# Kernel optimization log

Measured on AMD Instinct MI355X. Metric: run time of the kernel, lower is better.

## Reference

```python
import jax, jax.numpy as jnp
import numpy as np

B, T = 256, 1024
IN_DIM, OUT_DIM = 32, 32
STATE_DIM, DIM_NL = 128, 128
EPS = 1e-3            # pos_def_tol
ALPHA = 1.0           # contraction_rate_lb
STD = 0.5             # initialization_std


def setup_inputs() -> dict:
    key = jax.random.key(0)
    ks = jax.random.split(key, 9)
    f = lambda k, sh: jax.random.normal(k, sh, dtype=jnp.float32)
    n, q = STATE_DIM, DIM_NL
    return {
        "x0_sys": f(ks[0], (B, 1, OUT_DIM)),
        "u_in": f(ks[1], (B, T, IN_DIM)),
        "X": f(ks[2], (2 * n + q, 2 * n + q)) * STD,
        "Y": f(ks[3], (n, n)) * STD,
        "B2": f(ks[4], (n, IN_DIM)) * STD,
        "C2": f(ks[5], (OUT_DIM, n)) * STD,
        "D21": f(ks[6], (OUT_DIM, q)) * STD,
        "D22": f(ks[7], (OUT_DIM, IN_DIM)) * STD,
        "D12": f(ks[8], (q, IN_DIM)) * STD,
    }


def _derived(X, Y):
    # Contraction-preserving reparametrization ("_update_model_param").
    n, q = STATE_DIM, DIM_NL
    H = X.T @ X + EPS * jnp.eye(2 * n + q, dtype=X.dtype)
    H11 = H[:n, :n]
    H21 = H[n:n + q, :n]
    H22 = H[n:n + q, n:n + q]
    H31 = H[n + q:, :n]
    H32 = H[n + q:, n:n + q]
    H33 = H[n + q:, n + q:]          # P
    F_ = H31
    B1 = H32
    E = 0.5 * (H11 + ALPHA * H33 + Y - Y.T)
    E_inv = jnp.linalg.inv(E)
    Lam = 0.5 * jnp.diag(H22)
    D11 = -jnp.tril(H22, -1)          # strictly lower triangular
    C1 = -H21
    return F_, B1, E_inv, Lam, D11, C1


def reference(x0_sys, u_in, X, Y, B2, C2, D21, D22, D12):
    F_, B1, E_inv, Lam, D11, C1 = _derived(X, Y)
    q = DIM_NL

    # reset(): x0 = min-norm lstsq solution of C2 x0 = y0_sys  (lstsq == pinv here)
    y0_sys = x0_sys[:, 0, :]                       # (B, out)
    x0 = (jnp.linalg.pinv(C2) @ y0_sys.T).T        # (B, n)
    y0 = x0 @ C2.T                                 # (B, out)

    idx = jnp.arange(q)

    def step(x, u):
        # one REN forward step; x:(B,n), u:(B,in)
        a = x @ C1.T + u @ D12.T                   # (B, q), i-independent part of v

        def inner(w, inp):
            i, d_row, lam, a_i = inp               # a_i:(B,)
            v = a_i + w @ d_row                    # strictly-lower-tri recurrence on w
            return w.at[:, i].set(jnp.tanh(v / lam)), None

        w0 = jnp.zeros((x.shape[0], q), x.dtype)
        w, _ = jax.lax.scan(inner, w0, (idx, D11, Lam, a.T))
        x_new = (x @ F_.T + w @ B1.T + u @ B2.T) @ E_inv.T
        y = x_new @ C2.T + w @ D21.T + u @ D22.T
        return x_new, y

    _, ys = jax.lax.scan(step, x0, jnp.swapaxes(u_in, 0, 1))   # (T, B, out)
    # run() emits y0 then outputs after u[0..T-2] (last step's y is dropped)
    y_traj = jnp.concatenate([y0[None], ys[:-1]], axis=0)      # (T, B, out)
    return jnp.swapaxes(y_traj, 0, 1)                          # (B, T, out)
```

## Files before the change

### kernel.cpp

```cpp
#include <hip/hip_runtime.h>
#include <hip/hip_bf16.h>

#define DEV static __device__ __forceinline__

constexpr int Tn = 1024;
constexpr float LOG2E = 1.4426950408889634f;

constexpr int OFF_H     = 0;
constexpr int OFF_E     = 147456;
constexpr int OFF_EINV  = 163840;
constexpr int OFF_M     = 180224;
constexpr int OFF_MINV  = 181248;
constexpr int OFF_GL2   = 182272;
constexpr int OFF_FH    = 182400;
constexpr int OFF_B1H   = 198784;
constexpr int OFF_B2H   = 215168;
constexpr int OFF_W0    = 219264;
constexpr int OFF_WC    = 223360;
constexpr int OFF_CF    = 227456;
constexpr int OFF_CB    = 243840;
constexpr int OFF_CB2   = 260224;
constexpr int OFF_PF    = 264320;
constexpr int OFF_PB    = 280704;
constexpr int OFF_PCF   = 297088;
constexpr int OFF_PCB   = 313472;
constexpr int OFF_SAB   = 329856;
constexpr int OFF_SB2   = 338048;
constexpr int OFF_BUQ   = 342144;
constexpr int OFF_D12Q  = 346240;
constexpr int OFF_SCB2  = 350336;
constexpr int OFF_WCS   = 354432;
constexpr int OFF_C2Y   = 358528;
constexpr int OFF_D21Y  = 362624;
constexpr int OFF_D22Y  = 366720;
constexpr int OFF_AUG   = 367744;
constexpr int OFF_AUG2  = 400512;
constexpr int OFF_X0    = 402560;
constexpr int OFF_A0    = 435328;
constexpr int WS_FLOATS = 468096;

__device__ __align__(16) float g_ws[WS_FLOATS];
__device__ int g_isf32;

DEV float ld(const void* p, size_t i, int f) {
  return f ? ((const float*)p)[i]
           : __bfloat162float(((const __hip_bfloat16*)p)[i]);
}
DEV float rdlane(float v, int l) {
  return __int_as_float(__builtin_amdgcn_readlane(__float_as_int(v), l));
}

__global__ void k_detect(const void* __restrict__ X) {
  if (threadIdx.x == 0) {
    const __hip_bfloat16* p = (const __hip_bfloat16*)X;
    int bad = 0;
    for (int i = 0; i < 512; ++i) {
      float v = __bfloat162float(p[i]);
      if (!(v > -1e6f && v < 1e6f)) bad++;
    }
    g_isf32 = (bad > 0) ? 1 : 0;
  }
}

__global__ void k_H(const void* __restrict__ X) {
  const int f = g_isf32;
  float* ws = g_ws;
  int id = blockIdx.x * 256 + threadIdx.x;
  int r = id / 384, c = id % 384;
  float acc = 0.f;
  for (int k = 0; k < 384; ++k)
    acc = fmaf(ld(X, k * 384 + r, f), ld(X, k * 384 + c, f), acc);
  if (r == c) acc += 0.001f;
  ws[OFF_H + id] = acc;
}

__global__ void k_derived(const void* __restrict__ Y, const void* __restrict__ C2) {
  const int f = g_isf32;
  float* ws = g_ws;
  const float* H = ws + OFF_H;
  int id = blockIdx.x * 256 + threadIdx.x;
  if (id < 16384) {
    int i = id >> 7, j = id & 127;
    ws[OFF_E + id] = 0.5f * (H[i * 384 + j] + H[(256 + i) * 384 + 256 + j]
                             + ld(Y, i * 128 + j, f) - ld(Y, j * 128 + i, f));
  } else if (id < 16512) {
    int i = id - 16384;
    ws[OFF_GL2 + i] = LOG2E * 4.f / H[(128 + i) * 384 + 128 + i];
  } else if (id < 17536) {
    int t = id - 16512; int a = t >> 5, b = t & 31;
    float acc = 0.f;
    for (int j = 0; j < 128; ++j)
      acc = fmaf(ld(C2, a * 128 + j, f), ld(C2, b * 128 + j, f), acc);
// ... 121 lines not shown
  if (id < 16384) {
    int l = id >> 7, j = id & 127;
    float a = 0.f;
    for (int m = 0; m < 128; ++m) a = fmaf(einv[l * 128 + m], H[(256 + m) * 384 + j], a);
    ws[OFF_FH + id] = a;
  } else if (id < 32768) {
    int t = id - 16384; int l = t >> 7, j = t & 127;
    float a = 0.f;
    for (int m = 0; m < 128; ++m) a = fmaf(einv[l * 128 + m], H[(256 + m) * 384 + 128 + j], a);
    ws[OFF_B1H + t] = a;
  } else if (id < 36864) {
    int t = id - 32768; int l = t >> 5, k = t & 31;
    float a = 0.f;
    for (int m = 0; m < 128; ++m) a = fmaf(einv[l * 128 + m], ld(B2, m * 32 + k, f), a);
    ws[OFF_B2H + t] = a;
  } else if (id < 40960) {
    int t = id - 36864; int k = t >> 7, l = t & 127;
    float a = 0.f;
    for (int m = 0; m < 32; ++m) a = fmaf(minv[k * 32 + m], ld(C2, m * 128 + l, f), a);
    ws[OFF_W0 + t] = a;
  }
}

__global__ void k_w2() {
  float* ws = g_ws;
  const float* H = ws + OFF_H;
  const float* w0 = ws + OFF_W0;
  int id = blockIdx.x * 256 + threadIdx.x;
  int k = id >> 7, l = id & 127;
  float a = 0.f;
  for (int m = 0; m < 128; ++m) a = fmaf(w0[k * 128 + m], -H[(128 + l) * 384 + m], a);
  ws[OFF_WC + id] = a;
}

__global__ void k_cf() {
  float* ws = g_ws;
  const float* H = ws + OFF_H;
  int id = blockIdx.x * 256 + threadIdx.x;
  if (id < 16384) {
    int l = id >> 7, j = id & 127;
    float a = 0.f;
    for (int m = 0; m < 128; ++m) a = fmaf(-H[(128 + l) * 384 + m], ws[OFF_FH + m * 128 + j], a);
    ws[OFF_CF + id] = a;
  } else if (id < 32768) {
    int t = id - 16384; int l = t >> 7, j = t & 127;
    float a = 0.f;
    for (int m = 0; m < 128; ++m) a = fmaf(-H[(128 + l) * 384 + m], ws[OFF_B1H + m * 128 + j], a);
    ws[OFF_CB + t] = a;
  } else {
    int t = id - 32768; int l = t >> 5, k = t & 31;
    float a = 0.f;
    for (int m = 0; m < 128; ++m) a = fmaf(-H[(128 + l) * 384 + m], ws[OFF_B2H + m * 32 + k], a);
    ws[OFF_CB2 + t] = a;
  }
}

__global__ void k_pk(const void* __restrict__ D12, const void* __restrict__ C2,
                     const void* __restrict__ D21, const void* __restrict__ D22) {
  const int f = g_isf32;
  float* ws = g_ws;
  const float* H = ws + OFF_H;
  const float* g = ws + OFF_GL2;
  int id = blockIdx.x * 256 + threadIdx.x;
  if (id < 8192) {
    int j = id >> 6, l = id & 63;
    ((float2*)(ws + OFF_PF))[id] =
        make_float2(ws[OFF_FH + l * 128 + j], ws[OFF_FH + (l + 64) * 128 + j]);
  } else if (id < 16384) {
    int t = id - 8192; int j = t >> 6, l = t & 63;
    ((float2*)(ws + OFF_PB))[t] =
        make_float2(ws[OFF_B1H + l * 128 + j], ws[OFF_B1H + (l + 64) * 128 + j]);
  } else if (id < 24576) {
    int t = id - 16384; int j = t >> 6, l = t & 63;
    ((float2*)(ws + OFF_PCF))[t] =
        make_float2(g[l] * ws[OFF_CF + l * 128 + j], g[l + 64] * ws[OFF_CF + (l + 64) * 128 + j]);
  } else if (id < 32768) {
    int t = id - 24576; int j = t >> 6, l = t & 63;
    ((float2*)(ws + OFF_PCB))[t] =
        make_float2(g[l] * ws[OFF_CB + l * 128 + j], g[l + 64] * ws[OFF_CB + (l + 64) * 128 + j]);
  } else if (id < 36864) {
    int t = id - 32768; int i = t >> 6, l = t & 63;
    float sx = (i < l) ? -g[l] * H[(128 + l) * 384 + 128 + i] : 0.f;
    float sy = -g[l + 64] * H[(192 + l) * 384 + 128 + i];
    ((float2*)(ws + OFF_SAB))[t] = make_float2(sx, sy);
  } else if (id < 40960) {
    int t = id - 36864; int ii = t >> 6, l = t & 63;
    ws[OFF_SB2 + t] = (ii < l) ? -g[l + 64] * H[(192 + l) * 384 + 192 + ii] : 0.f;
  } else if (id < 43008) {
    int t = id - 40960; int k = t >> 6, l = t & 63;
    ((float2*)(ws + OFF_BUQ))[t] =
        make_float2(ws[OFF_B2H + l * 32 + k], ws[OFF_B2H + (l + 64) * 32 + k]);
  } else if (id < 45056) {
    int t = id - 43008; int k = t >> 6, l = t & 63;
    ((float2*)(ws + OFF_D12Q))[t] =
        make_float2(g[l] * ld(D12, l * 32 + k, f), g[l + 64] * ld(D12, (l + 64) * 32 + k, f));
  } else if (id < 47104) {
    int t = id - 45056; int k = t >> 6, l = t & 63;
    ((float2*)(ws + OFF_SCB2))[t] =
        make_float2(g[l] * ws[OFF_CB2 + l * 32 + k], g[l + 64] * ws[OFF_CB2 + (l + 64) * 32 + k]);
  } else if (id < 49152) {
    int t = id - 47104; int k = t >> 6, l = t & 63;
    ((float2*)(ws + OFF_WCS))[t] =
        make_float2(g[l] * ws[OFF_WC + k * 128 + l], g[l + 64] * ws[OFF_WC + k * 128 + l + 64]);
  } else if (id < 53248) {
    int t = id - 49152; int m = t >> 5, o = t & 31;
    ws[OFF_C2Y + t] = ld(C2, o * 128 + m, f);
  } else if (id < 57344) {
    int t = id - 53248; int m = t >> 5, o = t & 31;
    ws[OFF_D21Y + t] = ld(D21, o * 128 + m, f);
  } else if (id < 58368) {
    int t = id - 57344; int k = t >> 5, o = t & 31;
    ws[OFF_D22Y + t] = ld(D22, o * 32 + k, f);
  }
}

__global__ void k_x0a0(const void* __restrict__ x0s, const void* __restrict__ u_in) {
  const int f = g_isf32;
  float* ws = g_ws;
  int id = blockIdx.x * 256 + threadIdx.x;
  if (id < 32768) {
    int b = id >> 7, l = id & 127;
    float a = 0.f;
    for (int k = 0; k < 32; ++k)
      a = fmaf(ld(x0s, b * 32 + k, f), ws[OFF_W0 + k * 128 + l], a);
    ws[OFF_X0 + id] = a;
  } else {
    int t = id - 32768; int b = t >> 6, lane = t & 63;
    const float2* WCs = (const float2*)(ws + OFF_WCS);
    const float2* D12Q = (const float2*)(ws + OFF_D12Q);
    float ax = 0.f, ay = 0.f;
    for (int k = 0; k < 32; ++k) {
      float yk = ld(x0s, b * 32 + k, f);
      float2 wc = WCs[k * 64 + lane];
      ax = fmaf(wc.x, yk, ax); ay = fmaf(wc.y, yk, ay);
      float u0 = ld(u_in, b * Tn * 32 + k, f);
      float2 dq = D12Q[k * 64 + lane];
      ax = fmaf(dq.x, u0, ax); ay = fmaf(dq.y, u0, ay);
    }
    ((float2*)(ws + OFF_A0))[b * 64 + lane] = make_float2(ax, ay);
  }
}

DEV void y_emit(const float* ws, float xlv, float xhv, float2 wv, float uyv,
                int b, int t, int lane, int f, void* out) {
  int o = lane & 31, h = lane >> 5;
  const float* C2Y = ws + OFF_C2Y;
  const float* D21Y = ws + OFF_D21Y;
  const float* D22Y = ws + OFF_D22Y;
  float acc = 0.f;
#pragma unroll 8
  for (int l = 0; l < 64; ++l) {
    float xle = rdlane(xlv, l), xhe = rdlane(xhv, l);
    float xv = h ? xhe : xle;
    acc = fmaf(xv, C2Y[(l + 64 * h) * 32 + o], acc);
  }
#pragma unroll 8
  for (int l = 0; l < 64; ++l) {
    float wxe = rdlane(wv.x, l), wye = rdlane(wv.y, l);
    float wvv = h ? wye : wxe;
    acc = fmaf(wvv, D21Y[(l + 64 * h) * 32 + o], acc);
  }
  if (h == 0) {
#pragma unroll 8
    for (int k = 0; k < 32; ++k)
      acc = fmaf(rdlane(uyv, k), D22Y[k * 32 + o], acc);
  }
  acc += __shfl_down(acc, 32);
  if (lane < 32) {
    size_t oi = ((size_t)b * Tn + t) * 32 + o;
    if (f) ((float*)out)[oi] = acc;
    else   ((__hip_bfloat16*)out)[oi] = __float2bfloat16(acc);
  }
}

DEV void y_emit_l(const float* sC2Y, const float* sD21Y, const float* sD22Y,
                  float xlv, float xhv, float2 wv, float uyv,
                  int b, int t, int lane, int f, void* out) {
  int o = lane & 31, h = lane >> 5;
  float acc = 0.f;
#pragma unroll 8
  for (int l = 0; l < 64; ++l) {
    float xle = rdlane(xlv, l), xhe = rdlane(xhv, l);
    float xv = h ? xhe : xle;
    acc = fmaf(xv, sC2Y[(l + 64 * h) * 32 + o], acc);
  }
#pragma unroll 8
  for (int l = 0; l < 64; ++l) {
    float wxe = rdlane(wv.x, l), wye = rdlane(wv.y, l);
    float wvv = h ? wye : wxe;
    acc = fmaf(wvv, sD21Y[(l + 64 * h) * 32 + o], acc);
  }
  if (h == 0) {
#pragma unroll 8
    for (int k = 0; k < 32; ++k)
      acc = fmaf(rdlane(uyv, k), sD22Y[k * 32 + o], acc);
  }
  acc += __shfl_down(acc, 32);
  if (lane < 32) {
    size_t oi = ((size_t)b * Tn + t) * 32 + o;
    if (f) ((float*)out)[oi] = acc;
    else   ((__hip_bfloat16*)out)[oi] = __float2bfloat16(acc);
  }
}

__global__ __launch_bounds__(512, 2) void k_scan8m(const void* __restrict__ u_in,
                                                   const void* __restrict__ x0s,
                                                   void* __restrict__ out) {
  extern __shared__ float sm[];
  float2* sSAB  = (float2*)sm;
  float*  sSB2  = sm + 8192;
  float2* xbuf  = (float2*)(sm + 12288);
  float2* abuf  = (float2*)(sm + 14336);
  float2* wbuf  = (float2*)(sm + 16384);
  float2* sBUQ  = (float2*)(sm + 16640);
  float2* sSCB2 = (float2*)(sm + 20736);
  float2* sD12Q = (float2*)(sm + 24832);
  float*  sC2Y  = sm + 28928;
  float*  sD21Y = sm + 33024;
  float*  sD22Y = sm + 37120;
  const float* ws = g_ws;
  const int f = g_isf32;
  const int tid = threadIdx.x, lane = tid & 63, w = tid >> 6;
  for (int i = tid; i < 4096; i += 512) sSAB[i] = ((const float2*)(ws + OFF_SAB))[i];
  for (int i = tid; i < 4096; i += 512) sSB2[i] = ws[OFF_SB2 + i];
  for (int i = tid; i < 2048; i += 512) sBUQ[i] = ((const float2*)(ws + OFF_BUQ))[i];
  for (int i = tid; i < 2048; i += 512) sSCB2[i] = ((const float2*)(ws + OFF_SCB2))[i];
  for (int i = tid; i < 2048; i += 512) sD12Q[i] = ((const float2*)(ws + OFF_D12Q))[i];
  for (int i = tid; i < 4096; i += 512) sC2Y[i] = ws[OFF_C2Y + i];
  for (int i = tid; i < 4096; i += 512) sD21Y[i] = ws[OFF_D21Y + i];
  for (int i = tid; i < 1024; i += 512) sD22Y[i] = ws[OFF_D22Y + i];

  const int b = blockIdx.x;
  const bool isScan = (w < 4);

  float2 vA[32], vB[32];
  {
    const float2* P1 = (const float2*)(ws + (isScan ? OFF_PB : OFF_PF));
    const float2* P2 = (const float2*)(ws + (isScan ? OFF_PCB : OFF_PCF));
    const int jcol = (w & 3) * 32;
#pragma unroll
    for (int c = 0; c < 32; ++c) {
      vA[c] = P1[(jcol + c) * 64 + lane];
      vB[c] = P2[(jcol + c) * 64 + lane];
    }
  }
  float xl = ws[OFF_X0 + b * 128 + lane];
  float xh = ws[OFF_X0 + b * 128 + 64 + lane];
  float accx = 0.f, accy = 0.f;
  if (isScan) {
    float2 a2 = ((const float2*)(ws + OFF_A0))[b * 64 + lane];
    accx = a2.x; accy = a2.y;
  }
  float ucur = 0.f;
  float u0v = 0.f, u1v = 0.f;
  float uyc = 0.f;
  if (w == 4 && lane < 32) ucur = ld(u_in, (size_t)b * Tn * 32 + lane, f);
  if (w == 5 && lane < 32) {
    u0v = ld(u_in, (size_t)b * Tn * 32 + lane, f);
    u1v = ld(u_in, ((size_t)b * Tn + 1) * 32 + lane, f);
  }
  if (w == 7 && lane < 32) {
    size_t oi = (size_t)b * Tn * 32 + lane;
    float v = ld(x0s, b * 32 + lane, f);
    if (f) ((float*)out)[oi] = v;
    else   ((__hip_bfloat16*)out)[oi] = __float2bfloat16(v);
  }
  const int jb = __builtin_amdgcn_readfirstlane((w & 1) * 32);
  __syncthreads();

#pragma unroll 1
  for (int t = 0; t < Tn - 1; ++t) {
    const int p = t & 1;
    if (isScan) {
      __builtin_amdgcn_s_setprio(1);
      float s = rdlane(accx, 0);
#pragma unroll
      for (int i = 0; i < 64; ++i) {
        float e2 = __builtin_amdgcn_exp2f(s);
        float r  = __builtin_amdgcn_rcpf(1.f + e2);
        float wi = fmaf(-2.f, r, 1.f);
        float2 sp = sSAB[i * 64 + lane];
        if (i < 63) {
          float spn  = rdlane(sp.x, i + 1);
          float sold = rdlane(accx, i + 1);
          s = fmaf(spn, wi, sold);
        }
        accx = fmaf(sp.x, wi, accx);
        accy = fmaf(sp.y, wi, accy);
      }
      float ex = __builtin_amdgcn_exp2f(accx);
      float wxv = fmaf(-2.f, __builtin_amdgcn_rcpf(1.f + ex), 1.f);
      float s2 = rdlane(accy, 0);
#pragma unroll
      for (int i = 0; i < 64; ++i) {
        float e2 = __builtin_amdgcn_exp2f(s2);
        float r  = __builtin_amdgcn_rcpf(1.f + e2);
        float wi = fmaf(-2.f, r, 1.f);
        float sb = sSB2[i * 64 + lane];
        if (i < 63) {
          float spn  = rdlane(sb, i + 1);
          float sold = rdlane(accy, i + 1);
          s2 = fmaf(spn, wi, sold);
        }
        accy = fmaf(sb, wi, accy);
      }
      float ey = __builtin_amdgcn_exp2f(accy);
      float wyv = fmaf(-2.f, __builtin_amdgcn_rcpf(1.f + ey), 1.f);
      if (w == 0) wbuf[p * 64 + lane] = make_float2(wxv, wyv);

      float px = 0.f, py = 0.f, pax = 0.f, pay = 0.f;
      float wsrc = (w < 2) ? wxv : wyv;
#pragma unroll
      for (int c = 0; c < 32; ++c) {
        float wj = rdlane(wsrc, jb + c);
        px  = fmaf(vA[c].x, wj, px);
        py  = fmaf(vA[c].y, wj, py);
        pax = fmaf(vB[c].x, wj, pax);
        pay = fmaf(vB[c].y, wj, pay);
      }
      __builtin_amdgcn_s_setprio(0);
      xbuf[(p * 8 + w) * 64 + lane] = make_float2(px, py);
      abuf[(p * 8 + w) * 64 + lane] = make_float2(pax, pay);
      __syncthreads();
      float sax = 0.f, say = 0.f;
#pragma unroll
      for (int w2 = 0; w2 < 8; ++w2) {
        float2 av = abuf[(p * 8 + w2) * 64 + lane];
        sax += av.x; say += av.y;
      }
      accx = sax; accy = say;
    } else {
      float px = 0.f, py = 0.f, pax = 0.f, pay = 0.f;
      if (w == 4) {
        float un = ucur;
        if (lane < 32) un = ld(u_in, ((size_t)b * Tn + t + 1) * 32 + lane, f);
#pragma unroll 8
        for (int k = 0; k < 32; ++k) {
          float uk = rdlane(ucur, k);
          float2 bu = sBUQ[k * 64 + lane];
          px = fmaf(bu.x, uk, px); py = fmaf(bu.y, uk, py);
        }
        ucur = un;
      } else if (w == 5) {
        float u2v = u1v;
        if (lane < 32 && t + 2 < Tn) u2v = ld(u_in, ((size_t)b * Tn + t + 2) * 32 + lane, f);
#pragma unroll 8
        for (int k = 0; k < 32; ++k) {
          float u0k = rdlane(u0v, k);
          float2 sc = sSCB2[k * 64 + lane];
          pax = fmaf(sc.x, u0k, pax); pay = fmaf(sc.y, u0k, pay);
          float u1k = rdlane(u1v, k);
          float2 dq = sD12Q[k * 64 + lane];
          pax = fmaf(dq.x, u1k, pax); pay = fmaf(dq.y, u1k, pay);
        }
        u0v = u1v; u1v = u2v;
      } else if (w == 7) {
        float uyn = uyc;
        if (lane < 32) uyn = ld(u_in, ((size_t)b * Tn + t) * 32 + lane, f);
        if (t >= 1) {
          float2 wv = wbuf[((t - 1) & 1) * 64 + lane];
          y_emit_l(sC2Y, sD21Y, sD22Y, xl, xh, wv, uyc, b, t, lane, f, out);
        }
        uyc = uyn;
      }
      float xsrc = (w < 6) ? xl : xh;
#pragma unroll
      for (int c = 0; c < 32; ++c) {
        float xj = rdlane(xsrc, jb + c);
        px  = fmaf(vA[c].x, xj, px);
        py  = fmaf(vA[c].y, xj, py);
        pax = fmaf(vB[c].x, xj, pax);
        pay = fmaf(vB[c].y, xj, pay);
      }
      xbuf[(p * 8 + w) * 64 + lane] = make_float2(px, py);
      abuf[(p * 8 + w) * 64 + lane] = make_float2(pax, pay);
      __syncthreads();
      float sxl = 0.f, sxh = 0.f;
#pragma unroll
      for (int w2 = 0; w2 < 8; ++w2) {
        float2 xv = xbuf[(p * 8 + w2) * 64 + lane];
        sxl += xv.x; sxh += xv.y;
      }
      xl = sxl; xh = sxh;
    }
  }
  if (w == 7) {
    float2 wv = wbuf[((Tn - 2) & 1) * 64 + lane];
    y_emit_l(sC2Y, sD21Y, sD22Y, xl, xh, wv, uyc, b, Tn - 1, lane, f, out);
  }
}

__global__ __launch_bounds__(512) void k_scan8_fb(const void* __restrict__ u_in,
                                                  const void* __restrict__ x0s,
                                                  void* __restrict__ out) {
  __shared__ float2 sSAB[64 * 64];
  __shared__ float  sSB2[64 * 64];
  __shared__ float2 xbuf[2][8][64];
  __shared__ float2 abuf[2][8][64];
  const float* ws = g_ws;
  const int f = g_isf32;
  const int tid = threadIdx.x, lane = tid & 63, w = tid >> 6;
  for (int i = tid; i < 4096; i += 512) sSAB[i] = ((const float2*)(ws + OFF_SAB))[i];
  for (int i = tid; i < 4096; i += 512) sSB2[i] = ws[OFF_SB2 + i];

  const int b = blockIdx.x;
  const bool isScan = (w < 4);
  float2 vA[32], vB[32];
  if (isScan) {
    const float2* P1 = (const float2*)(ws + OFF_PB);
    const float2* P2 = (const float2*)(ws + OFF_PCB);
    const int jcol = (w & 3) * 32;
#pragma unroll
    for (int c = 0; c < 32; ++c) {
      vA[c] = P1[(jcol + c) * 64 + lane];
      vB[c] = P2[(jcol + c) * 64 + lane];
    }
  }
  float xl = ws[OFF_X0 + b * 128 + lane];
  float xh = ws[OFF_X0 + b * 128 + 64 + lane];
  float2 a2 = ((const float2*)(ws + OFF_A0))[b * 64 + lane];
  float accx = a2.x, accy = a2.y;
  float ucur = 0.f;
  float u0v = 0.f, u1v = 0.f;
  float uyc = 0.f;
  if (w == 4 && lane < 32) ucur = ld(u_in, (size_t)b * Tn * 32 + lane, f);
  if (w == 6 && lane < 32) {
    u0v = ld(u_in, (size_t)b * Tn * 32 + lane, f);
    u1v = ld(u_in, ((size_t)b * Tn + 1) * 32 + lane, f);
  }
  if (w == 6) { xbuf[0][6][lane] = make_float2(0.f, 0.f); xbuf[1][6][lane] = make_float2(0.f, 0.f); }
  if (w == 7 && lane < 32) {
    size_t oi = (size_t)b * Tn * 32 + lane;
    float v = ld(x0s, b * 32 + lane, f);
    if (f) ((float*)out)[oi] = v;
    else   ((__hip_bfloat16*)out)[oi] = __float2bfloat16(v);
  }
  const int jb = __builtin_amdgcn_readfirstlane((w & 1) * 32);
  __syncthreads();

#pragma unroll 1
  for (int t = 0; t < Tn - 1; ++t) {
// ... 77 lines not shown
      xl = sxl; xh = sxh;
    } else if (w == 5) {
      float px = 0.f, py = 0.f, pax = 0.f, pay = 0.f;
      const float2* PF = (const float2*)(ws + OFF_PF);
      const float2* PCF = (const float2*)(ws + OFF_PCF);
#pragma unroll 8
      for (int c = 0; c < 64; ++c) {
        float xj = rdlane(xh, c);
        float2 fv = PF[(64 + c) * 64 + lane];
        float2 cv = PCF[(64 + c) * 64 + lane];
        px  = fmaf(fv.x, xj, px);  py  = fmaf(fv.y, xj, py);
        pax = fmaf(cv.x, xj, pax); pay = fmaf(cv.y, xj, pay);
      }
      xbuf[p][5][lane] = make_float2(px, py);
      abuf[p][5][lane] = make_float2(pax, pay);
      __syncthreads();
      float sxl = 0.f, sxh = 0.f;
#pragma unroll
      for (int w2 = 0; w2 < 7; ++w2) {
        float2 xv = xbuf[p][w2][lane];
        sxl += xv.x; sxh += xv.y;
      }
      xl = sxl; xh = sxh;
    } else if (w == 6) {
      float u2v = u1v;
      if (lane < 32 && t + 2 < Tn) u2v = ld(u_in, ((size_t)b * Tn + t + 2) * 32 + lane, f);
      float pax = 0.f, pay = 0.f;
      const float2* SC = (const float2*)(ws + OFF_SCB2);
      const float2* DQ = (const float2*)(ws + OFF_D12Q);
#pragma unroll 8
      for (int k = 0; k < 32; ++k) {
        float u0k = rdlane(u0v, k);
        float2 sc = SC[k * 64 + lane];
        pax = fmaf(sc.x, u0k, pax); pay = fmaf(sc.y, u0k, pay);
        float u1k = rdlane(u1v, k);
        float2 dq = DQ[k * 64 + lane];
        pax = fmaf(dq.x, u1k, pax); pay = fmaf(dq.y, u1k, pay);
      }
      u0v = u1v; u1v = u2v;
      abuf[p][6][lane] = make_float2(pax, pay);
      __syncthreads();
      float sxl = 0.f, sxh = 0.f;
#pragma unroll
      for (int w2 = 0; w2 < 7; ++w2) {
        float2 xv = xbuf[p][w2][lane];
        sxl += xv.x; sxh += xv.y;
      }
      xl = sxl; xh = sxh;
    } else {
      float uyn = uyc;
      if (lane < 32) uyn = ld(u_in, ((size_t)b * Tn + t) * 32 + lane, f);
      if (t >= 1) {
        float2 wv = xbuf[(t - 1) & 1][7][lane];
        y_emit(ws, xl, xh, wv, uyc, b, t, lane, f, out);
      }
      uyc = uyn;
      __syncthreads();
      float sxl = 0.f, sxh = 0.f;
#pragma unroll
      for (int w2 = 0; w2 < 7; ++w2) {
        float2 xv = xbuf[p][w2][lane];
        sxl += xv.x; sxh += xv.y;
      }
      xl = sxl; xh = sxh;
    }
  }
  if (w == 7) {
    float2 wv = xbuf[(Tn - 2) & 1][7][lane];
    y_emit(ws, xl, xh, wv, uyc, b, Tn - 1, lane, f, out);
  }
}

extern "C" void kernel_launch(void* const* d_in, const int* in_sizes, int n_in,
                              void* d_out, int out_size, void* d_ws, size_t ws_size,
                              hipStream_t stream) {
  const void* x0s = d_in[0];
  const void* u   = d_in[1];
  const void* X   = d_in[2];
  const void* Y   = d_in[3];
  const void* B2  = d_in[4];
  const void* C2  = d_in[5];
  const void* D21 = d_in[6];
  const void* D22 = d_in[7];
  const void* D12 = d_in[8];
  (void)d_ws; (void)ws_size; (void)in_sizes; (void)n_in; (void)out_size;

  hipLaunchKernelGGL(k_detect,  dim3(1),     dim3(64),   0, stream, X);
  hipLaunchKernelGGL(k_H,       dim3(576),   dim3(256),  0, stream, X);
  hipLaunchKernelGGL(k_derived, dim3(69),    dim3(256),  0, stream, Y, C2);

  hipError_t e = hipFuncSetAttribute((const void*)k_inv_lds,
                                     hipFuncAttributeMaxDynamicSharedMemorySize,
                                     139264);
  if (e == hipSuccess) {
    hipLaunchKernelGGL(k_inv_lds, dim3(1), dim3(1024), 139264, stream);
  } else {
    (void)hipGetLastError();
    hipLaunchKernelGGL(k_inv,     dim3(1), dim3(1024), 0, stream);
  }

  hipLaunchKernelGGL(k_fuse,    dim3(160),   dim3(256),  0, stream, B2, C2);
  hipLaunchKernelGGL(k_w2,      dim3(16),    dim3(256),  0, stream);
  hipLaunchKernelGGL(k_cf,      dim3(144),   dim3(256),  0, stream);
  hipLaunchKernelGGL(k_pk,      dim3(228),   dim3(256),  0, stream, D12, C2, D21, D22);
  hipLaunchKernelGGL(k_x0a0,    dim3(192),   dim3(256),  0, stream, x0s, u);

  hipError_t e2 = hipFuncSetAttribute((const void*)k_scan8m,
                                      hipFuncAttributeMaxDynamicSharedMemorySize,
                                      152576);
  if (e2 == hipSuccess) {
    hipLaunchKernelGGL(k_scan8m, dim3(256), dim3(512), 152576, stream, u, x0s, d_out);
  } else {
    (void)hipGetLastError();
    hipLaunchKernelGGL(k_scan8_fb, dim3(256), dim3(512), 0, stream, u, x0s, d_out);
  }
}
```

Baseline: 6.940 ms.

## Fold w-dependent terms into precomputed matrices so scan waves split critical path

Precomputes the products F·B1, CF·B1 and C2·B1+D21 so the state update and next-step pre-activation can be formed directly from the previous step's w and x. This lets the four non-scan waves compute the whole x update, while the scan waves only handle the w recurrence and its contribution to a, shortening the serial critical path. Weights move from registers into LDS or are streamed from global memory, trading register pressure and occupancy for extra memory traffic. The launch-bounds minimum-occupancy hint is removed and the LDS allocation shrinks.

```diff
diff --git a/kernel.cpp b/kernel.cpp
--- a/kernel.cpp
+++ b/kernel.cpp
@@ -37,7 +37,12 @@
 constexpr int OFF_AUG2  = 400512;
 constexpr int OFF_X0    = 402560;
 constexpr int OFF_A0    = 435328;
-constexpr int WS_FLOATS = 468096;
+constexpr int OFF_M1    = 468096;
+constexpr int OFF_M2    = 484480;
+constexpr int OFF_M3Y   = 500864;
+constexpr int OFF_PM1   = 504960;
+constexpr int OFF_PM2   = 521344;
+constexpr int WS_FLOATS = 537728;
 
 __device__ __align__(16) float g_ws[WS_FLOATS];
 __device__ int g_isf32;
@@ -265,6 +270,31 @@
     float a = 0.f;
     for (int m = 0; m < 128; ++m) a = fmaf(-H[(128 + l) * 384 + m], ws[OFF_B2H + m * 32 + k], a);
     ws[OFF_CB2 + t] = a;
+  }
+}
+
+__global__ void k_m(const void* __restrict__ C2, const void* __restrict__ D21) {
+  const int f = g_isf32;
+  float* ws = g_ws;
+  int id = blockIdx.x * 256 + threadIdx.x;
+  if (id < 16384) {
+    int l = id >> 7, j = id & 127;
+    float a = 0.f;
+    for (int m = 0; m < 128; ++m)
+      a = fmaf(ws[OFF_FH + l * 128 + m], ws[OFF_B1H + m * 128 + j], a);
+    ws[OFF_M1 + id] = a;
+  } else if (id < 32768) {
+    int t = id - 16384; int l = t >> 7, j = t & 127;
+    float a = 0.f;
+    for (int m = 0; m < 128; ++m)
+      a = fmaf(ws[OFF_CF + l * 128 + m], ws[OFF_B1H + m * 128 + j], a);
+    ws[OFF_M2 + t] = a;
+  } else {
+    int t = id - 32768; int m = t >> 5, o = t & 31;
+    float a = ld(D21, o * 128 + m, f);
+    for (int l = 0; l < 128; ++l)
+      a = fmaf(ld(C2, o * 128 + l, f), ws[OFF_B1H + l * 128 + m], a);
+    ws[OFF_M3Y + t] = a;
   }
 }
 
@@ -324,6 +354,14 @@
   } else if (id < 58368) {
     int t = id - 57344; int k = t >> 5, o = t & 31;
     ws[OFF_D22Y + t] = ld(D22, o * 32 + k, f);
+  } else if (id < 66560) {
+    int t = id - 58368; int j = t >> 6, l = t & 63;
+    ((float2*)(ws + OFF_PM1))[t] =
+        make_float2(ws[OFF_M1 + l * 128 + j], ws[OFF_M1 + (l + 64) * 128 + j]);
+  } else if (id < 74752) {
+    int t = id - 66560; int j = t >> 6, l = t & 63;
+    ((float2*)(ws + OFF_PM2))[t] =
+        make_float2(g[l] * ws[OFF_M2 + l * 128 + j], g[l + 64] * ws[OFF_M2 + (l + 64) * 128 + j]);
   }
 }
 
@@ -354,12 +392,10 @@
   }
 }
 
-DEV void y_emit(const float* ws, float xlv, float xhv, float2 wv, float uyv,
-                int b, int t, int lane, int f, void* out) {
+DEV void y_emit_p(const float* C2Y, const float* DY, const float* D22Y,
+                  float xlv, float xhv, float2 wv, float uyv,
+                  int b, int t, int lane, int f, void* out) {
   int o = lane & 31, h = lane >> 5;
-  const float* C2Y = ws + OFF_C2Y;
-  const float* D21Y = ws + OFF_D21Y;
-  const float* D22Y = ws + OFF_D22Y;
   float acc = 0.f;
 #pragma unroll 8
   for (int l = 0; l < 64; ++l) {
@@ -371,7 +407,7 @@
   for (int l = 0; l < 64; ++l) {
     float wxe = rdlane(wv.x, l), wye = rdlane(wv.y, l);
     float wvv = h ? wye : wxe;
-    acc = fmaf(wvv, D21Y[(l + 64 * h) * 32 + o], acc);
+    acc = fmaf(wvv, DY[(l + 64 * h) * 32 + o], acc);
   }
   if (h == 0) {
 #pragma unroll 8
@@ -386,77 +422,27 @@
   }
 }
 
-DEV void y_emit_l(const float* sC2Y, const float* sD21Y, const float* sD22Y,
-                  float xlv, float xhv, float2 wv, float uyv,
-                  int b, int t, int lane, int f, void* out) {
-  int o = lane & 31, h = lane >> 5;
-  float acc = 0.f;
-#pragma unroll 8
-  for (int l = 0; l < 64; ++l) {
-    float xle = rdlane(xlv, l), xhe = rdlane(xhv, l);
-    float xv = h ? xhe : xle;
-    acc = fmaf(xv, sC2Y[(l + 64 * h) * 32 + o], acc);
-  }
-#pragma unroll 8
-  for (int l = 0; l < 64; ++l) {
-    float wxe = rdlane(wv.x, l), wye = rdlane(wv.y, l);
-    float wvv = h ? wye : wxe;
-    acc = fmaf(wvv, sD21Y[(l + 64 * h) * 32 + o], acc);
-  }
-  if (h == 0) {
-#pragma unroll 8
-    for (int k = 0; k < 32; ++k)
-      acc = fmaf(rdlane(uyv, k), sD22Y[k * 32 + o], acc);
-  }
-  acc += __shfl_down(acc, 32);
-  if (lane < 32) {
-    size_t oi = ((size_t)b * Tn + t) * 32 + o;
-    if (f) ((float*)out)[oi] = acc;
-    else   ((__hip_bfloat16*)out)[oi] = __float2bfloat16(acc);
-  }
-}
-
-__global__ __launch_bounds__(512, 2) void k_scan8m(const void* __restrict__ u_in,
-                                                   const void* __restrict__ x0s,
-                                                   void* __restrict__ out) {
+__global__ __launch_bounds__(512) void k_scan9(const void* __restrict__ u_in,
+                                               const void* __restrict__ x0s,
+                                               void* __restrict__ out) {
   extern __shared__ float sm[];
-  float2* sSAB  = (float2*)sm;
-  float*  sSB2  = sm + 8192;
-  float2* xbuf  = (float2*)(sm + 12288);
-  float2* abuf  = (float2*)(sm + 14336);
-  float2* wbuf  = (float2*)(sm + 16384);
-  float2* sBUQ  = (float2*)(sm + 16640);
-  float2* sSCB2 = (float2*)(sm + 20736);
-  float2* sD12Q = (float2*)(sm + 24832);
-  float*  sC2Y  = sm + 28928;
-  float*  sD21Y = sm + 33024;
-  float*  sD22Y = sm + 37120;
+  float2* sSAB = (float2*)sm;
+  float*  sSB2 = sm + 8192;
+  float2* sPCB = (float2*)(sm + 12288);
+  float2* xbuf = (float2*)(sm + 28672);
+  float2* abuf = (float2*)(sm + 30720);
+  float2* wbuf = (float2*)(sm + 32768);
   const float* ws = g_ws;
   const int f = g_isf32;
   const int tid = threadIdx.x, lane = tid & 63, w = tid >> 6;
   for (int i = tid; i < 4096; i += 512) sSAB[i] = ((const float2*)(ws + OFF_SAB))[i];
   for (int i = tid; i < 4096; i += 512) sSB2[i] = ws[OFF_SB2 + i];
-  for (int i = tid; i < 2048; i += 512) sBUQ[i] = ((const float2*)(ws + OFF_BUQ))[i];
-  for (int i = tid; i < 2048; i += 512) sSCB2[i] = ((const float2*)(ws + OFF_SCB2))[i];
-  for (int i = tid; i < 2048; i += 512) sD12Q[i] = ((const float2*)(ws + OFF_D12Q))[i];
-  for (int i = tid; i < 4096; i += 512) sC2Y[i] = ws[OFF_C2Y + i];
-  for (int i = tid; i < 4096; i += 512) sD21Y[i] = ws[OFF_D21Y + i];
-  for (int i = tid; i < 1024; i += 512) sD22Y[i] = ws[OFF_D22Y + i];
+  for (int i = tid; i < 8192; i += 512) sPCB[i] = ((const float2*)(ws + OFF_PCB))[i];
+  if (tid < 128) wbuf[tid] = make_float2(0.f, 0.f);
 
   const int b = blockIdx.x;
   const bool isScan = (w < 4);
 
-  float2 vA[32], vB[32];
-  {
-    const float2* P1 = (const float2*)(ws + (isScan ? OFF_PB : OFF_PF));
-    const float2* P2 = (const float2*)(ws + (isScan ? OFF_PCB : OFF_PCF));
-    const int jcol = (w & 3) * 32;
-#pragma unroll
-    for (int c = 0; c < 32; ++c) {
-      vA[c] = P1[(jcol + c) * 64 + lane];
-      vB[c] = P2[(jcol + c) * 64 + lane];
-    }
-  }
   float xl = ws[OFF_X0 + b * 128 + lane];
   float xh = ws[OFF_X0 + b * 128 + 64 + lane];
   float accx = 0.f, accy = 0.f;
@@ -521,18 +507,17 @@
       float wyv = fmaf(-2.f, __builtin_amdgcn_rcpf(1.f + ey), 1.f);
       if (w == 0) wbuf[p * 64 + lane] = make_float2(wxv, wyv);
 
-      float px = 0.f, py = 0.f, pax = 0.f, pay = 0.f;
+      float pax = 0.f, pay = 0.f;
       float wsrc = (w < 2) ? wxv : wyv;
+      const int jcol = w * 32;
 #pragma unroll
       for (int c = 0; c < 32; ++c) {
         float wj = rdlane(wsrc, jb + c);
-        px  = fmaf(vA[c].x, wj, px);
-        py  = fmaf(vA[c].y, wj, py);
-        pax = fmaf(vB[c].x, wj, pax);
-        pay = fmaf(vB[c].y, wj, pay);
+        float2 cv = sPCB[(jcol + c) * 64 + lane];
+        pax = fmaf(cv.x, wj, pax);
+        pay = fmaf(cv.y, wj, pay);
       }
       __builtin_amdgcn_s_setprio(0);
-      xbuf[(p * 8 + w) * 64 + lane] = make_float2(px, py);
       abuf[(p * 8 + w) * 64 + lane] = make_float2(pax, pay);
       __syncthreads();
       float sax = 0.f, say = 0.f;
@@ -543,27 +528,31 @@
       }
       accx = sax; accy = say;
     } else {
+      float2 wprev = wbuf[(p ^ 1) * 64 + lane];
       float px = 0.f, py = 0.f, pax = 0.f, pay = 0.f;
       if (w == 4) {
         float un = ucur;
         if (lane < 32) un = ld(u_in, ((size_t)b * Tn + t + 1) * 32 + lane, f);
+        const float2* BUq = (const float2*)(ws + OFF_BUQ);
 #pragma unroll 8
         for (int k = 0; k < 32; ++k) {
           float uk = rdlane(ucur, k);
-          float2 bu = sBUQ[k * 64 + lane];
+          float2 bu = BUq[k * 64 + lane];
           px = fmaf(bu.x, uk, px); py = fmaf(bu.y, uk, py);
         }
         ucur = un;
       } else if (w == 5) {
         float u2v = u1v;
         if (lane < 32 && t + 2 < Tn) u2v = ld(u_in, ((size_t)b * Tn + t + 2) * 32 + lane, f);
+        const float2* SC = (const float2*)(ws + OFF_SCB2);
+        const float2* DQ = (const float2*)(ws + OFF_D12Q);
 #pragma unroll 8
         for (int k = 0; k < 32; ++k) {
           float u0k = rdlane(u0v, k);
-          float2 sc = sSCB2[k * 64 + lane];
+          float2 sc = SC[k * 64 + lane];
           pax = fmaf(sc.x, u0k, pax); pay = fmaf(sc.y, u0k, pay);
           float u1k = rdlane(u1v, k);
-          float2 dq = sD12Q[k * 64 + lane];
+          float2 dq = DQ[k * 64 + lane];
           pax = fmaf(dq.x, u1k, pax); pay = fmaf(dq.y, u1k, pay);
         }
         u0v = u1v; u1v = u2v;
@@ -571,26 +560,37 @@
         float uyn = uyc;
         if (lane < 32) uyn = ld(u_in, ((size_t)b * Tn + t) * 32 + lane, f);
         if (t >= 1) {
-          float2 wv = wbuf[((t - 1) & 1) * 64 + lane];
-          y_emit_l(sC2Y, sD21Y, sD22Y, xl, xh, wv, uyc, b, t, lane, f, out);
+          y_emit_p(ws + OFF_C2Y, ws + OFF_M3Y, ws + OFF_D22Y,
+                   xl, xh, wprev, uyc, b, t, lane, f, out);
         }
         uyc = uyn;
       }
       float xsrc = (w < 6) ? xl : xh;
-#pragma unroll
+      float wps  = (w < 6) ? wprev.x : wprev.y;
+      const int jc = (w - 4) * 32;
+      const float2* PFp  = (const float2*)(ws + OFF_PF);
+      const float2* PM1p = (const float2*)(ws + OFF_PM1);
+      const float2* PCFp = (const float2*)(ws + OFF_PCF);
+      const float2* PM2p = (const float2*)(ws + OFF_PM2);
+#pragma unroll 8
       for (int c = 0; c < 32; ++c) {
         float xj = rdlane(xsrc, jb + c);
-        px  = fmaf(vA[c].x, xj, px);
-        py  = fmaf(vA[c].y, xj, py);
-        pax = fmaf(vB[c].x, xj, pax);
-        pay = fmaf(vB[c].y, xj, pay);
+        float wj = rdlane(wps, jb + c);
+        float2 fv = PFp [(jc + c) * 64 + lane];
+        float2 mv = PM1p[(jc + c) * 64 + lane];
+        float2 cv = PCFp[(jc + c) * 64 + lane];
+        float2 nv = PM2p[(jc + c) * 64 + lane];
+        px  = fmaf(fv.x, xj, px);  py  = fmaf(fv.y, xj, py);
+        px  = fmaf(mv.x, wj, px);  py  = fmaf(mv.y, wj, py);
+        pax = fmaf(cv.x, xj, pax); pay = fmaf(cv.y, xj, pay);
+        pax = fmaf(nv.x, wj, pax); pay = fmaf(nv.y, wj, pay);
       }
       xbuf[(p * 8 + w) * 64 + lane] = make_float2(px, py);
       abuf[(p * 8 + w) * 64 + lane] = make_float2(pax, pay);
       __syncthreads();
       float sxl = 0.f, sxh = 0.f;
 #pragma unroll
-      for (int w2 = 0; w2 < 8; ++w2) {
+      for (int w2 = 4; w2 < 8; ++w2) {
         float2 xv = xbuf[(p * 8 + w2) * 64 + lane];
         sxl += xv.x; sxh += xv.y;
       }
@@ -599,7 +599,8 @@
   }
   if (w == 7) {
     float2 wv = wbuf[((Tn - 2) & 1) * 64 + lane];
-    y_emit_l(sC2Y, sD21Y, sD22Y, xl, xh, wv, uyc, b, Tn - 1, lane, f, out);
+    y_emit_p(ws + OFF_C2Y, ws + OFF_M3Y, ws + OFF_D22Y,
+             xl, xh, wv, uyc, b, Tn - 1, lane, f, out);
   }
 }
 
@@ -783,7 +784,8 @@
       if (lane < 32) uyn = ld(u_in, ((size_t)b * Tn + t) * 32 + lane, f);
       if (t >= 1) {
         float2 wv = xbuf[(t - 1) & 1][7][lane];
-        y_emit(ws, xl, xh, wv, uyc, b, t, lane, f, out);
+        y_emit_p(ws + OFF_C2Y, ws + OFF_D21Y, ws + OFF_D22Y,
+                 xl, xh, wv, uyc, b, t, lane, f, out);
       }
       uyc = uyn;
       __syncthreads();
@@ -798,7 +800,8 @@
   }
   if (w == 7) {
     float2 wv = xbuf[(Tn - 2) & 1][7][lane];
-    y_emit(ws, xl, xh, wv, uyc, b, Tn - 1, lane, f, out);
+    y_emit_p(ws + OFF_C2Y, ws + OFF_D21Y, ws + OFF_D22Y,
+             xl, xh, wv, uyc, b, Tn - 1, lane, f, out);
   }
 }
 
@@ -833,14 +836,15 @@
   hipLaunchKernelGGL(k_fuse,    dim3(160),   dim3(256),  0, stream, B2, C2);
   hipLaunchKernelGGL(k_w2,      dim3(16),    dim3(256),  0, stream);
   hipLaunchKernelGGL(k_cf,      dim3(144),   dim3(256),  0, stream);
-  hipLaunchKernelGGL(k_pk,      dim3(228),   dim3(256),  0, stream, D12, C2, D21, D22);
+  hipLaunchKernelGGL(k_m,       dim3(144),   dim3(256),  0, stream, C2, D21);
+  hipLaunchKernelGGL(k_pk,      dim3(292),   dim3(256),  0, stream, D12, C2, D21, D22);
   hipLaunchKernelGGL(k_x0a0,    dim3(192),   dim3(256),  0, stream, x0s, u);
 
-  hipError_t e2 = hipFuncSetAttribute((const void*)k_scan8m,
+  hipError_t e2 = hipFuncSetAttribute((const void*)k_scan9,
                                       hipFuncAttributeMaxDynamicSharedMemorySize,
-                                      152576);
+                                      132096);
   if (e2 == hipSuccess) {
-    hipLaunchKernelGGL(k_scan8m, dim3(256), dim3(512), 152576, stream, u, x0s, d_out);
+    hipLaunchKernelGGL(k_scan9, dim3(256), dim3(512), 132096, stream, u, x0s, d_out);
   } else {
     (void)hipGetLastError();
     hipLaunchKernelGGL(k_scan8_fb, dim3(256), dim3(512), 0, stream, u, x0s, d_out);
```

Measured after the change: 14.97 ms. +115.7%, slower.

## Split scan block into 16 specialized waves with separate x-update and input waves

Applied to the files above, without the earlier changes.

The per-batch scan kernel grows from 8 to 16 waves per block. Four waves run the serial tanh chain, eight waves compute the state projection with 16 columns each, and dedicated waves handle the input projections and output emission. Those helper tasks previously ran alongside the x-projection on the same waves. The aim is to shorten the non-chain critical path each timestep. In exchange the 14-way reductions are larger, the block is bigger with one block per CU instead of two, and the projection weights are now read from global memory each step rather than kept in registers.

```diff
diff --git a/kernel.cpp b/kernel.cpp
--- a/kernel.cpp
+++ b/kernel.cpp
@@ -354,39 +354,7 @@
   }
 }
 
-DEV void y_emit(const float* ws, float xlv, float xhv, float2 wv, float uyv,
-                int b, int t, int lane, int f, void* out) {
-  int o = lane & 31, h = lane >> 5;
-  const float* C2Y = ws + OFF_C2Y;
-  const float* D21Y = ws + OFF_D21Y;
-  const float* D22Y = ws + OFF_D22Y;
-  float acc = 0.f;
-#pragma unroll 8
-  for (int l = 0; l < 64; ++l) {
-    float xle = rdlane(xlv, l), xhe = rdlane(xhv, l);
-    float xv = h ? xhe : xle;
-    acc = fmaf(xv, C2Y[(l + 64 * h) * 32 + o], acc);
-  }
-#pragma unroll 8
-  for (int l = 0; l < 64; ++l) {
-    float wxe = rdlane(wv.x, l), wye = rdlane(wv.y, l);
-    float wvv = h ? wye : wxe;
-    acc = fmaf(wvv, D21Y[(l + 64 * h) * 32 + o], acc);
-  }
-  if (h == 0) {
-#pragma unroll 8
-    for (int k = 0; k < 32; ++k)
-      acc = fmaf(rdlane(uyv, k), D22Y[k * 32 + o], acc);
-  }
-  acc += __shfl_down(acc, 32);
-  if (lane < 32) {
-    size_t oi = ((size_t)b * Tn + t) * 32 + o;
-    if (f) ((float*)out)[oi] = acc;
-    else   ((__hip_bfloat16*)out)[oi] = __float2bfloat16(acc);
-  }
-}
-
-DEV void y_emit_l(const float* sC2Y, const float* sD21Y, const float* sD22Y,
+DEV void y_emit_p(const float* C2Y, const float* DY, const float* D22Y,
                   float xlv, float xhv, float2 wv, float uyv,
                   int b, int t, int lane, int f, void* out) {
   int o = lane & 31, h = lane >> 5;
@@ -395,18 +363,18 @@
   for (int l = 0; l < 64; ++l) {
     float xle = rdlane(xlv, l), xhe = rdlane(xhv, l);
     float xv = h ? xhe : xle;
-    acc = fmaf(xv, sC2Y[(l + 64 * h) * 32 + o], acc);
+    acc = fmaf(xv, C2Y[(l + 64 * h) * 32 + o], acc);
   }
 #pragma unroll 8
   for (int l = 0; l < 64; ++l) {
     float wxe = rdlane(wv.x, l), wye = rdlane(wv.y, l);
     float wvv = h ? wye : wxe;
-    acc = fmaf(wvv, sD21Y[(l + 64 * h) * 32 + o], acc);
+    acc = fmaf(wvv, DY[(l + 64 * h) * 32 + o], acc);
   }
   if (h == 0) {
 #pragma unroll 8
     for (int k = 0; k < 32; ++k)
-      acc = fmaf(rdlane(uyv, k), sD22Y[k * 32 + o], acc);
+      acc = fmaf(rdlane(uyv, k), D22Y[k * 32 + o], acc);
   }
   acc += __shfl_down(acc, 32);
   if (lane < 32) {
@@ -416,41 +384,41 @@
   }
 }
 
-__global__ __launch_bounds__(512, 2) void k_scan8m(const void* __restrict__ u_in,
-                                                   const void* __restrict__ x0s,
-                                                   void* __restrict__ out) {
+__global__ __launch_bounds__(1024) void k_scan16(const void* __restrict__ u_in,
+                                                 const void* __restrict__ x0s,
+                                                 void* __restrict__ out) {
   extern __shared__ float sm[];
   float2* sSAB  = (float2*)sm;
   float*  sSB2  = sm + 8192;
   float2* xbuf  = (float2*)(sm + 12288);
-  float2* abuf  = (float2*)(sm + 14336);
-  float2* wbuf  = (float2*)(sm + 16384);
-  float2* sBUQ  = (float2*)(sm + 16640);
-  float2* sSCB2 = (float2*)(sm + 20736);
-  float2* sD12Q = (float2*)(sm + 24832);
-  float*  sC2Y  = sm + 28928;
-  float*  sD21Y = sm + 33024;
-  float*  sD22Y = sm + 37120;
+  float2* abuf  = (float2*)(sm + 16384);
+  float2* wbuf  = (float2*)(sm + 20480);
+  float*  sC2Y  = sm + 20736;
+  float*  sD21Y = sm + 24832;
+  float*  sD22Y = sm + 28928;
   const float* ws = g_ws;
   const int f = g_isf32;
   const int tid = threadIdx.x, lane = tid & 63, w = tid >> 6;
-  for (int i = tid; i < 4096; i += 512) sSAB[i] = ((const float2*)(ws + OFF_SAB))[i];
-  for (int i = tid; i < 4096; i += 512) sSB2[i] = ws[OFF_SB2 + i];
-  for (int i = tid; i < 2048; i += 512) sBUQ[i] = ((const float2*)(ws + OFF_BUQ))[i];
-  for (int i = tid; i < 2048; i += 512) sSCB2[i] = ((const float2*)(ws + OFF_SCB2))[i];
-  for (int i = tid; i < 2048; i += 512) sD12Q[i] = ((const float2*)(ws + OFF_D12Q))[i];
-  for (int i = tid; i < 4096; i += 512) sC2Y[i] = ws[OFF_C2Y + i];
-  for (int i = tid; i < 4096; i += 512) sD21Y[i] = ws[OFF_D21Y + i];
-  for (int i = tid; i < 1024; i += 512) sD22Y[i] = ws[OFF_D22Y + i];
+  for (int i = tid; i < 4096; i += 1024) sSAB[i] = ((const float2*)(ws + OFF_SAB))[i];
+  for (int i = tid; i < 4096; i += 1024) sSB2[i] = ws[OFF_SB2 + i];
+  for (int i = tid; i < 4096; i += 1024) sC2Y[i] = ws[OFF_C2Y + i];
+  for (int i = tid; i < 4096; i += 1024) sD21Y[i] = ws[OFF_D21Y + i];
+  if (tid < 1024) { if (tid < 1024) sD22Y[tid] = ws[OFF_D22Y + tid]; }
+  if (tid < 64) {
+    xbuf[(0 * 16 + 13) * 64 + tid] = make_float2(0.f, 0.f);
+    xbuf[(1 * 16 + 13) * 64 + tid] = make_float2(0.f, 0.f);
+    abuf[(0 * 16 + 12) * 64 + tid] = make_float2(0.f, 0.f);
+    abuf[(1 * 16 + 12) * 64 + tid] = make_float2(0.f, 0.f);
+  }
 
   const int b = blockIdx.x;
-  const bool isScan = (w < 4);
+  const bool isChain = (w < 4);
 
   float2 vA[32], vB[32];
-  {
-    const float2* P1 = (const float2*)(ws + (isScan ? OFF_PB : OFF_PF));
-    const float2* P2 = (const float2*)(ws + (isScan ? OFF_PCB : OFF_PCF));
-    const int jcol = (w & 3) * 32;
+  if (isChain) {
+    const float2* P1 = (const float2*)(ws + OFF_PB);
+    const float2* P2 = (const float2*)(ws + OFF_PCB);
+    const int jcol = w * 32;
 #pragma unroll
     for (int c = 0; c < 32; ++c) {
       vA[c] = P1[(jcol + c) * 64 + lane];
@@ -460,31 +428,32 @@
   float xl = ws[OFF_X0 + b * 128 + lane];
   float xh = ws[OFF_X0 + b * 128 + 64 + lane];
   float accx = 0.f, accy = 0.f;
-  if (isScan) {
+  if (isChain) {
     float2 a2 = ((const float2*)(ws + OFF_A0))[b * 64 + lane];
     accx = a2.x; accy = a2.y;
   }
   float ucur = 0.f;
   float u0v = 0.f, u1v = 0.f;
   float uyc = 0.f;
-  if (w == 4 && lane < 32) ucur = ld(u_in, (size_t)b * Tn * 32 + lane, f);
-  if (w == 5 && lane < 32) {
+  if (w == 12 && lane < 32) ucur = ld(u_in, (size_t)b * Tn * 32 + lane, f);
+  if (w == 13 && lane < 32) {
     u0v = ld(u_in, (size_t)b * Tn * 32 + lane, f);
     u1v = ld(u_in, ((size_t)b * Tn + 1) * 32 + lane, f);
   }
-  if (w == 7 && lane < 32) {
+  if (w == 14 && lane < 32) {
     size_t oi = (size_t)b * Tn * 32 + lane;
     float v = ld(x0s, b * 32 + lane, f);
     if (f) ((float*)out)[oi] = v;
     else   ((__hip_bfloat16*)out)[oi] = __float2bfloat16(v);
   }
-  const int jb = __builtin_amdgcn_readfirstlane((w & 1) * 32);
+  const int jbC = __builtin_amdgcn_readfirstlane((w & 1) * 32);
+  const int jbX = __builtin_amdgcn_readfirstlane(((w - 4) & 3) * 16);
   __syncthreads();
 
 #pragma unroll 1
   for (int t = 0; t < Tn - 1; ++t) {
     const int p = t & 1;
-    if (isScan) {
+    if (isChain) {
       __builtin_amdgcn_s_setprio(1);
       float s = rdlane(accx, 0);
 #pragma unroll
@@ -525,81 +494,102 @@
       float wsrc = (w < 2) ? wxv : wyv;
 #pragma unroll
       for (int c = 0; c < 32; ++c) {
-        float wj = rdlane(wsrc, jb + c);
+        float wj = rdlane(wsrc, jbC + c);
         px  = fmaf(vA[c].x, wj, px);
         py  = fmaf(vA[c].y, wj, py);
         pax = fmaf(vB[c].x, wj, pax);
         pay = fmaf(vB[c].y, wj, pay);
       }
       __builtin_amdgcn_s_setprio(0);
-      xbuf[(p * 8 + w) * 64 + lane] = make_float2(px, py);
-      abuf[(p * 8 + w) * 64 + lane] = make_float2(pax, pay);
+      xbuf[(p * 16 + w) * 64 + lane] = make_float2(px, py);
+      abuf[(p * 16 + w) * 64 + lane] = make_float2(pax, pay);
       __syncthreads();
       float sax = 0.f, say = 0.f;
 #pragma unroll
-      for (int w2 = 0; w2 < 8; ++w2) {
-        float2 av = abuf[(p * 8 + w2) * 64 + lane];
+      for (int w2 = 0; w2 < 14; ++w2) {
+        float2 av = abuf[(p * 16 + w2) * 64 + lane];
         sax += av.x; say += av.y;
       }
       accx = sax; accy = say;
+    } else if (w < 12) {
+      float px = 0.f, py = 0.f, pax = 0.f, pay = 0.f;
+      float xsrc = (w < 8) ? xl : xh;
+      const int jc = (w - 4) * 16;
+      const float2* PF  = (const float2*)(ws + OFF_PF);
+      const float2* PCF = (const float2*)(ws + OFF_PCF);
+#pragma unroll
+      for (int c = 0; c < 16; ++c) {
+        float xj = rdlane(xsrc, jbX + c);
+        float2 fv = PF [(jc + c) * 64 + lane];
+        float2 cv = PCF[(jc + c) * 64 + lane];
+        px  = fmaf(fv.x, xj, px);  py  = fmaf(fv.y, xj, py);
+        pax = fmaf(cv.x, xj, pax); pay = fmaf(cv.y, xj, pay);
+      }
+      xbuf[(p * 16 + w) * 64 + lane] = make_float2(px, py);
+      abuf[(p * 16 + w) * 64 + lane] = make_float2(pax, pay);
+      __syncthreads();
+      float sxl = 0.f, sxh = 0.f;
+#pragma unroll
+      for (int w2 = 0; w2 < 14; ++w2) {
+        float2 xv = xbuf[(p * 16 + w2) * 64 + lane];
+        sxl += xv.x; sxh += xv.y;
+      }
+      xl = sxl; xh = sxh;
+    } else if (w == 12) {
+      float un = ucur;
+      if (lane < 32) un = ld(u_in, ((size_t)b * Tn + t + 1) * 32 + lane, f);
+      float px = 0.f, py = 0.f;
+      const float2* BUq = (const float2*)(ws + OFF_BUQ);
+#pragma unroll 8
+      for (int k = 0; k < 32; ++k) {
+        float uk = rdlane(ucur, k);
+        float2 bu = BUq[k * 64 + lane];
+        px = fmaf(bu.x, uk, px); py = fmaf(bu.y, uk, py);
+      }
+      ucur = un;
+      xbuf[(p * 16 + 12) * 64 + lane] = make_float2(px, py);
+      __syncthreads();
+    } else if (w == 13) {
+      float u2v = u1v;
+      if (lane < 32 && t + 2 < Tn) u2v = ld(u_in, ((size_t)b * Tn + t + 2) * 32 + lane, f);
+      float pax = 0.f, pay = 0.f;
+      const float2* SC = (const float2*)(ws + OFF_SCB2);
+      const float2* DQ = (const float2*)(ws + OFF_D12Q);
+#pragma unroll 8
+      for (int k = 0; k < 32; ++k) {
+        float u0k = rdlane(u0v, k);
+        float2 sc = SC[k * 64 + lane];
+        pax = fmaf(sc.x, u0k, pax); pay = fmaf(sc.y, u0k, pay);
+        float u1k = rdlane(u1v, k);
+        float2 dq = DQ[k * 64 + lane];
+        pax = fmaf(dq.x, u1k, pax); pay = fmaf(dq.y, u1k, pay);
+      }
+      u0v = u1v; u1v = u2v;
+      abuf[(p * 16 + 13) * 64 + lane] = make_float2(pax, pay);
+      __syncthreads();
+    } else if (w == 14) {
+      float uyn = uyc;
+      if (lane < 32) uyn = ld(u_in, ((size_t)b * Tn + t) * 32 + lane, f);
+      if (t >= 1) {
+        float2 wv = wbuf[((t - 1) & 1) * 64 + lane];
+        y_emit_p(sC2Y, sD21Y, sD22Y, xl, xh, wv, uyc, b, t, lane, f, out);
+      }
+      uyc = uyn;
+      __syncthreads();
+      float sxl = 0.f, sxh = 0.f;
+#pragma unroll
+      for (int w2 = 0; w2 < 14; ++w2) {
+        float2 xv = xbuf[(p * 16 + w2) * 64 + lane];
+        sxl += xv.x; sxh += xv.y;
+      }
+      xl = sxl; xh = sxh;
     } else {
-      float px = 0.f, py = 0.f, pax = 0.f, pay = 0.f;
-      if (w == 4) {
-        float un = ucur;
-        if (lane < 32) un = ld(u_in, ((size_t)b * Tn + t + 1) * 32 + lane, f);
-#pragma unroll 8
-        for (int k = 0; k < 32; ++k) {
-          float uk = rdlane(ucur, k);
-          float2 bu = sBUQ[k * 64 + lane];
-          px = fmaf(bu.x, uk, px); py = fmaf(bu.y, uk, py);
-        }
-        ucur = un;
-      } else if (w == 5) {
-        float u2v = u1v;
-        if (lane < 32 && t + 2 < Tn) u2v = ld(u_in, ((size_t)b * Tn + t + 2) * 32 + lane, f);
-#pragma unroll 8
-        for (int k = 0; k < 32; ++k) {
-          float u0k = rdlane(u0v, k);
-          float2 sc = sSCB2[k * 64 + lane];
-          pax = fmaf(sc.x, u0k, pax); pay = fmaf(sc.y, u0k, pay);
-          float u1k = rdlane(u1v, k);
-          float2 dq = sD12Q[k * 64 + lane];
-          pax = fmaf(dq.x, u1k, pax); pay = fmaf(dq.y, u1k, pay);
-        }
-        u0v = u1v; u1v = u2v;
-      } else if (w == 7) {
-        float uyn = uyc;
-        if (lane < 32) uyn = ld(u_in, ((size_t)b * Tn + t) * 32 + lane, f);
-        if (t >= 1) {
-          float2 wv = wbuf[((t - 1) & 1) * 64 + lane];
-          y_emit_l(sC2Y, sD21Y, sD22Y, xl, xh, wv, uyc, b, t, lane, f, out);
-        }
-        uyc = uyn;
-      }
-      float xsrc = (w < 6) ? xl : xh;
-#pragma unroll
-      for (int c = 0; c < 32; ++c) {
-        float xj = rdlane(xsrc, jb + c);
-        px  = fmaf(vA[c].x, xj, px);
-        py  = fmaf(vA[c].y, xj, py);
-        pax = fmaf(vB[c].x, xj, pax);
-        pay = fmaf(vB[c].y, xj, pay);
-      }
-      xbuf[(p * 8 + w) * 64 + lane] = make_float2(px, py);
-      abuf[(p * 8 + w) * 64 + lane] = make_float2(pax, pay);
-      __syncthreads();
-      float sxl = 0.f, sxh = 0.f;
-#pragma unroll
-      for (int w2 = 0; w2 < 8; ++w2) {
-        float2 xv = xbuf[(p * 8 + w2) * 64 + lane];
-        sxl += xv.x; sxh += xv.y;
-      }
-      xl = sxl; xh = sxh;
-    }
-  }
-  if (w == 7) {
+      __syncthreads();
+    }
+  }
+  if (w == 14) {
     float2 wv = wbuf[((Tn - 2) & 1) * 64 + lane];
-    y_emit_l(sC2Y, sD21Y, sD22Y, xl, xh, wv, uyc, b, Tn - 1, lane, f, out);
+    y_emit_p(sC2Y, sD21Y, sD22Y, xl, xh, wv, uyc, b, Tn - 1, lane, f, out);
   }
 }
 
@@ -783,7 +773,8 @@
       if (lane < 32) uyn = ld(u_in, ((size_t)b * Tn + t) * 32 + lane, f);
       if (t >= 1) {
         float2 wv = xbuf[(t - 1) & 1][7][lane];
-        y_emit(ws, xl, xh, wv, uyc, b, t, lane, f, out);
+        y_emit_p(ws + OFF_C2Y, ws + OFF_D21Y, ws + OFF_D22Y,
+                 xl, xh, wv, uyc, b, t, lane, f, out);
       }
       uyc = uyn;
       __syncthreads();
@@ -798,7 +789,8 @@
   }
   if (w == 7) {
     float2 wv = xbuf[(Tn - 2) & 1][7][lane];
-    y_emit(ws, xl, xh, wv, uyc, b, Tn - 1, lane, f, out);
+    y_emit_p(ws + OFF_C2Y, ws + OFF_D21Y, ws + OFF_D22Y,
+             xl, xh, wv, uyc, b, Tn - 1, lane, f, out);
   }
 }
 
@@ -836,11 +828,11 @@
   hipLaunchKernelGGL(k_pk,      dim3(228),   dim3(256),  0, stream, D12, C2, D21, D22);
   hipLaunchKernelGGL(k_x0a0,    dim3(192),   dim3(256),  0, stream, x0s, u);
 
-  hipError_t e2 = hipFuncSetAttribute((const void*)k_scan8m,
+  hipError_t e2 = hipFuncSetAttribute((const void*)k_scan16,
                                       hipFuncAttributeMaxDynamicSharedMemorySize,
-                                      152576);
+                                      119808);
   if (e2 == hipSuccess) {
-    hipLaunchKernelGGL(k_scan8m, dim3(256), dim3(512), 152576, stream, u, x0s, d_out);
+    hipLaunchKernelGGL(k_scan16, dim3(256), dim3(1024), 119808, stream, u, x0s, d_out);
   } else {
     (void)hipGetLastError();
     hipLaunchKernelGGL(k_scan8_fb, dim3(256), dim3(512), 0, stream, u, x0s, d_out);
```

Result: slower. 18.18 ms (+162.0%).
